# Kernel optimization log

Measured on AMD Instinct MI355X. Metric: run time of the kernel, lower is better.

## Reference

```python
import jax, jax.numpy as jnp
import numpy as np

N_NODES = 200000
N_EDGES = 800000
D_IN = 64
D_OUT = 64
NUM_RELATIONS = 16
NUM_BASES = 8


def setup_inputs() -> dict:
    key = jax.random.key(0)
    k_x, k_s, k_t, k_r, k_b, k_a = jax.random.split(key, 6)
    x = jax.random.normal(k_x, (N_NODES, D_IN), dtype=jnp.float32)
    node_keep_mask = jnp.ones((N_NODES,), dtype=bool)
    source = jax.random.randint(k_s, (N_EDGES,), 0, N_NODES, dtype=jnp.int64)
    target = jax.random.randint(k_t, (N_EDGES,), 0, N_NODES, dtype=jnp.int64)
    edge_type = jax.random.randint(k_r, (N_EDGES,), 0, NUM_RELATIONS, dtype=jnp.int64)
    # parameters: xavier-normal bases, L1-normalized attention coefficients
    std = float(np.sqrt(2.0 / (D_IN + D_OUT)))
    bases = jax.random.normal(k_b, (NUM_BASES, D_IN, D_OUT), dtype=jnp.float32) * std
    att = jax.random.uniform(k_a, (NUM_RELATIONS + 1, NUM_BASES), dtype=jnp.float32)
    att = att / jnp.sum(jnp.abs(att), axis=1, keepdims=True)
    return {"x": x, "node_keep_mask": node_keep_mask, "source": source,
            "target": target, "edge_type": edge_type, "bases": bases, "att": att}


def reference(x, node_keep_mask, source, target, edge_type, bases, att):
    num_relations = att.shape[0] - 1
    # per-node, per-basis transformed features: (N, B, D_out)
    t = jnp.einsum('nd,bde->nbe', x, bases)
    # self-loop term (att row num_relations), masked by node_keep_mask
    self_msg = jnp.einsum('nbe,b->ne', t, att[num_relations])
    out = jnp.where(node_keep_mask[:, None], self_msg, jnp.zeros((), dtype=x.dtype))
    # per-node, per-relation messages: (N, R, D_out) -- collapses the per-relation
    # python loop of the original into one contraction
    h = jnp.einsum('nbe,rb->nre', t, att[:num_relations])
    # bidirectional edges (original concatenates [src,tgt] and [tgt,src])
    src2 = jnp.concatenate([source, target])
    tgt2 = jnp.concatenate([target, source])
    et2 = jnp.concatenate([edge_type, edge_type])
    m = h[src2, et2]  # (2E, D_out) gather
    out = out.at[tgt2].add(m)  # scatter-add over edges
    return out
```

## Files before the change

kernel.cpp:

```cpp
#include <hip/hip_runtime.h>
#include <hip/hip_bf16.h>
#include <stdint.h>
#include <stddef.h>

#define N_NODES 200000
#define N_EDGES 800000
#define NREL 16
#define NBASES 8

typedef __attribute__((ext_vector_type(8))) short short8b;
typedef __attribute__((ext_vector_type(4))) float float4v;
typedef __attribute__((ext_vector_type(4))) int int4v;

__device__ __forceinline__ short f32_bf16(float f) {
  uint32_t u = __builtin_bit_cast(uint32_t, f);
  uint32_t r = u + 0x7FFFu + ((u >> 16) & 1u);
  return (short)(uint16_t)(r >> 16);
}
__device__ __forceinline__ uint16_t f32_bf16_hw(float f) {
  __hip_bfloat16 h = __float2bfloat16(f);
  return __builtin_bit_cast(uint16_t, h);
}
__device__ __forceinline__ float bf2f(uint16_t h) {
  return __builtin_bit_cast(float, (uint32_t)h << 16);
}

__global__ __launch_bounds__(256) void k_wprep(const float* __restrict__ bases,
                                               const float* __restrict__ att,
                                               uint16_t* __restrict__ Wt) {
  int i = blockIdx.x * 256 + threadIdx.x;
  if (i >= 17 * 64 * 64) return;
  int r = i >> 12;
  int e = (i >> 6) & 63;
  int d = i & 63;
  float acc = 0.f;
  for (int b = 0; b < NBASES; ++b)
    acc += att[r * NBASES + b] * bases[b * 4096 + d * 64 + e];
  Wt[i] = (uint16_t)f32_bf16(acc);
}

#define MAXTILES 112528
#define MAXRECS  (MAXTILES * 16)
#define NB 196
#define CNT_BLOCKS  782
#define CAST_BLOCKS 6250
#define WS_CNTR    0
#define WS_GCUR2   128
#define WS_RSTART  256
#define WS_GCUR    384
#define WS_WT      512
#define WS_TILEREL 139776
#define WS_CNTV    252416
#define WS_VSTART  1052416
#define WS_CNTT    1852416
#define WS_RECS    2652416
#define WS_MSG     17056128
#define WS_TOTAL   (WS_MSG + (size_t)MAXRECS * 128)
#define TR_RELOFF  WS_MSG
#define TR_NOFF    (TR_RELOFF + 3200000)
#define TR_ESLOT   (TR_NOFF + 800000)
#define TR_SCRATCH (TR_ESLOT + 6400000)
#define TR_H       (TR_SCRATCH + 6400000)
#define TR_BASE    (TR_H + 613088)
#define TR_REGS    (TR_BASE + 613088)

__global__ __launch_bounds__(256) void k_init(const float* __restrict__ bases,
                                              const float* __restrict__ att,
                                              uint16_t* __restrict__ Wt,
                                              int* __restrict__ zero0) {
  int b = blockIdx.x;
  int tid = threadIdx.x;
  if (b < 273) {
    int i = b * 256 + tid;
    if (i < 17 * 64 * 64) {
      int r = i >> 12;
      int e = (i >> 6) & 63;
      int d = i & 63;
      float acc = 0.f;
      for (int bb = 0; bb < NBASES; ++bb)
        acc += att[r * NBASES + bb] * bases[bb * 4096 + d * 64 + e];
      Wt[i] = (uint16_t)f32_bf16(acc);
    }
  } else {
    if (tid < 128) zero0[tid] = 0;
  }
}

__global__ __launch_bounds__(256) void k_count(const int* __restrict__ src,
                                               const int* __restrict__ tgt,
                                               const int* __restrict__ et,
                                               const int* __restrict__ mask,
                                               int* __restrict__ cntr,
                                               int* __restrict__ H,
                                               int* __restrict__ reloff,
                                               int* __restrict__ noff,
                                               const float* __restrict__ x,
                                               uint16_t* __restrict__ xb,
                                               int nE, int nN) {
  int b = blockIdx.x;
  int tid = threadIdx.x;
  if (b >= CNT_BLOCKS) {
    int i = (b - CNT_BLOCKS) * 256 + tid;
    const float* xp = x + (size_t)i * 8;
    float4v q0 = __builtin_nontemporal_load((const float4v*)xp);
    float4v q1 = __builtin_nontemporal_load((const float4v*)(xp + 4));
    short8b o;
    o[0] = f32_bf16_hw(q0[0]); o[1] = f32_bf16_hw(q0[1]); o[2] = f32_bf16_hw(q0[2]); o[3] = f32_bf16_hw(q0[3]);
    o[4] = f32_bf16_hw(q1[0]); o[5] = f32_bf16_hw(q1[1]); o[6] = f32_bf16_hw(q1[2]); o[7] = f32_bf16_hw(q1[3]);
    *(short8b*)(xb + (size_t)i * 8) = o;
    return;
  }
  __shared__ int lh[NREL + 1], lbase[NREL + 1];
  __shared__ int bh[NB];
  if (tid <= NREL) lh[tid] = 0;
  if (tid < NB) bh[tid] = 0;
  __syncthreads();
  int base = b * 1024 + tid;
  bool isE[4], isN[4];
  int r4[4], loff[4], loffN[4];
#pragma unroll
  for (int k = 0; k < 4; ++k) {
    int i = base + k * 256;
    isE[k] = i < nE;
    isN[k] = (i < nN) && mask[i];
    if (isE[k]) {
      r4[k] = et[i];
      int s_ = src[i], t_ = tgt[i];
      loff[k] = atomicAdd(&lh[r4[k]], 2);
      atomicAdd(&bh[t_ >> 10], 1);
      atomicAdd(&bh[s_ >> 10], 1);
    }
    if (isN[k]) loffN[k] = atomicAdd(&lh[NREL], 1);
  }
  __syncthreads();
  if (tid <= NREL)
    lbase[tid] = lh[tid] ? atomicAdd(&cntr[tid], lh[tid]) : 0;
  if (tid < NB) H[b * NB + tid] = bh[tid];
  __syncthreads();
#pragma unroll
  for (int k = 0; k < 4; ++k) {
    int i = base + k * 256;
    if (isE[k]) __builtin_nontemporal_store(lbase[r4[k]] + loff[k], reloff + i);
    if (isN[k]) __builtin_nontemporal_store(lbase[NREL] + loffN[k], noff + i);
  }
}

__global__ __launch_bounds__(256) void k_base(const int* __restrict__ H,
                                              int* __restrict__ baseM,
                                              int* __restrict__ regStart,
                                              int* __restrict__ regTot,
                                              int* __restrict__ gcur2) {
  int b = blockIdx.x;
  int tid = threadIdx.x;
  int lane = tid & 63, wid = tid >> 6;
  int vals[4]; int ts = 0;
#pragma unroll
  for (int k = 0; k < 4; ++k) {
    int idx = tid * 4 + k;
    vals[k] = (idx < CNT_BLOCKS) ? H[idx * NB + b] : 0;
    ts += vals[k];
  }
  int incl = ts;
  for (int off = 1; off < 64; off <<= 1) {
    int n = __shfl_up(incl, off, 64);
    if (lane >= off) incl += n;
  }
  __shared__ int wsum[4];
  __shared__ int s_start;
  if (lane == 63) wsum[wid] = incl;
  __syncthreads();
  if (tid == 0) {
    int t0 = wsum[0], t1 = wsum[1], t2 = wsum[2], t3 = wsum[3];
    int tot = t0 + t1 + t2 + t3;
    int st = atomicAdd(gcur2, tot);
    regStart[b] = st;
    regTot[b] = tot;
    s_start = st;
    wsum[0] = 0; wsum[1] = t0; wsum[2] = t0 + t1; wsum[3] = t0 + t1 + t2;
  }
  __syncthreads();
  int run = s_start + wsum[wid] + incl - ts;
#pragma unroll
  for (int k = 0; k < 4; ++k) {
    int idx = tid * 4 + k;
    if (idx < CNT_BLOCKS) {
      baseM[idx * NB + b] = run;
      run += vals[k];
    }
  }
}

__global__ __launch_bounds__(256) void k_scat(const int* __restrict__ src,
                                              const int* __restrict__ tgt,
                                              const int* __restrict__ baseM,
                                              int* __restrict__ scratch,
                                              int nE) {
  int b = blockIdx.x;
  int tid = threadIdx.x;
  __shared__ int bh[NB];
  __shared__ int bb[NB];
  if (tid < NB) { bh[tid] = 0; bb[tid] = baseM[b * NB + tid]; }
  __syncthreads();
#pragma unroll
  for (int k = 0; k < 4; ++k) {
    int i = b * 1024 + k * 256 + tid;
    if (i < nE) {
      int t_ = tgt[i], s_ = src[i];
      int offT = atomicAdd(&bh[t_ >> 10], 1);
      scratch[bb[t_ >> 10] + offT] = ((t_ & 1023) << 21) | (2 * i);
      int offS = atomicAdd(&bh[s_ >> 10], 1);
      scratch[bb[s_ >> 10] + offS] = ((s_ & 1023) << 21) | (2 * i + 1);
    }
  }
}

__global__ __launch_bounds__(256) void k_slot(const int* __restrict__ scratch,
                                              const int* __restrict__ regStart,
                                              const int* __restrict__ regTot,
                                              int* __restrict__ eslot,
                                              int* __restrict__ cntv,
                                              int nN) {
  int b = blockIdx.x;
  int tid = threadIdx.x;
  __shared__ int cnt[1024];
#pragma unroll
  for (int k = 0; k < 4; ++k) cnt[tid + k * 256] = 0;
  __syncthreads();
  int start = regStart[b];
  int tot = regTot[b];
  for (int it = tid; it < tot; it += 256) {
    int rec = scratch[start + it];
    int off = atomicAdd(&cnt[rec >> 21], 1);
    eslot[rec & 0x1FFFFF] = off;
  }
  __syncthreads();
#pragma unroll
  for (int k = 0; k < 4; ++k) {
    int v = b * 1024 + k * 256 + tid;
    if (v < nN) cntv[v] = cnt[k * 256 + tid];
  }
}

#define PREP_BLOCKS 440
#define VSEG_BLOCKS 782
__global__ __launch_bounds__(256) void k_scan(const int* __restrict__ cntr,
                                              int* __restrict__ rstart_g,
                                              uint8_t* __restrict__ tileRel,
                                              int2* __restrict__ recs,
                                              const int* __restrict__ cntv,
                                              const int* __restrict__ mask,
                                              int* __restrict__ vstart,
                                              int* __restrict__ cntt,
                                              int* __restrict__ gcur,
                                              int maxTiles, int nN) {
  int b = blockIdx.x;
  if (b < PREP_BLOCKS) {
    __shared__ int s[NREL + 2];
    if (threadIdx.x == 0) {
      int base = 0;
      for (int r = 0; r <= NREL; ++r) {
        s[r] = base;
        base = (base + cntr[r] + 15) & ~15;
      }
      s[NREL + 1] = base;
    }
    __syncthreads();
    if (b == 0) {
      if (threadIdx.x <= NREL + 1) rstart_g[threadIdx.x] = s[threadIdx.x];
      for (int w = threadIdx.x; w < (NREL + 1) * 16; w += 256) {
        int r = w >> 4, j = w & 15;
        int pos = s[r] + cntr[r] + j;
        if (pos < s[r + 1]) recs[pos] = make_int2(-1, -1);
      }
    }
    int t = b * 256 + threadIdx.x;
    if (t < maxTiles) {
      int p = t * 16;
      uint8_t rr = 255;
      if (p < s[NREL + 1]) {
        int q = 0;
        for (int k = 1; k <= NREL; ++k)
          if (p >= s[k]) q = k;
        rr = (uint8_t)q;
      }
      tileRel[t] = rr;
    }
  } else {
    __shared__ int wsum[4];
    __shared__ int s_base;
    int v = (b - PREP_BLOCKS) * 256 + threadIdx.x;
    int lane = threadIdx.x & 63;
    int wid = threadIdx.x >> 6;
    int c = 0;
    if (v < nN) c = cntv[v] + (mask[v] ? 1 : 0);
    int incl = c;
    for (int off = 1; off < 64; off <<= 1) {
      int n = __shfl_up(incl, off, 64);
      if (lane >= off) incl += n;
    }
    if (lane == 63) wsum[wid] = incl;
    __syncthreads();
    if (threadIdx.x == 0) {
      int t0 = wsum[0], t1 = wsum[1], t2 = wsum[2], t3 = wsum[3];
      s_base = atomicAdd(gcur, t0 + t1 + t2 + t3);
      wsum[0] = 0;
      wsum[1] = t0;
      wsum[2] = t0 + t1;
      wsum[3] = t0 + t1 + t2;
    }
    __syncthreads();
    if (v < nN) {
      vstart[v] = s_base + wsum[wid] + incl - c;
      cntt[v] = c;
    }
  }
}

__global__ __launch_bounds__(256) void k_write(const int* __restrict__ src,
                                               const int* __restrict__ tgt,
                                               const int* __restrict__ et,
                                               const int* __restrict__ mask,
                                               const int* __restrict__ reloff,
                                               const int* __restrict__ noff,
                                               const int* __restrict__ eslot,
                                               const int* __restrict__ rstart,
                                               const int* __restrict__ cntv,
                                               const int* __restrict__ vstart,
                                               int2* __restrict__ recs,
                                               int nE, int nN) {
  __shared__ int s_rs[NREL + 1];
  if (threadIdx.x <= NREL) s_rs[threadIdx.x] = rstart[threadIdx.x];
  __syncthreads();
  int i = blockIdx.x * 256 + threadIdx.x;
  if (i < nE) {
    int r = et[i];
    int rl = __builtin_nontemporal_load(reloff + i);
    long long ev = __builtin_nontemporal_load((const long long*)(eslot + 2 * i));
    int o1 = (int)(ev & 0xFFFFFFFFll);
    int o2 = (int)(ev >> 32);
    int s_ = src[i], t_ = tgt[i];
    int pos = s_rs[r] + rl;
    int s1 = vstart[t_] + o1;
    int s2 = vstart[s_] + o2;
    *(int4*)(recs + pos) = make_int4(s_, s1, t_, s2);
  }
  if (i < nN && mask[i]) {
    int pos = s_rs[NREL] + noff[i];
    int slot = vstart[i] + cntv[i];
    recs[pos] = make_int2(i, slot);
  }
}

__global__ __launch_bounds__(256) void k_phaseA(const uint16_t* __restrict__ xb,
                                                const int2* __restrict__ recs,
                                                const uint16_t* __restrict__ Wt,
                                                const uint8_t* __restrict__ tileRel,
                                                uint16_t* __restrict__ msg,
                                                int ntiles) {
  __shared__ uint16_t s_m[4][16 * 72];
  __shared__ int s_slot[4][16];
  const int wid = threadIdx.x >> 6;
  const int lane = threadIdx.x & 63;
  const int quad = lane >> 4;
  const int m16 = lane & 15;
  const int t0 = (blockIdx.x * 4 + wid) * 4;

  if (tileRel[t0] == 255) return;

  int rel4[4];
#pragma unroll
  for (int it = 0; it < 4; ++it) {
    int t = t0 + it;
    rel4[it] = (t < ntiles) ? (int)tileRel[t] : 255;
  }
  int2 rec4[4];
#pragma unroll
  for (int it = 0; it < 4; ++it) {
    if (rel4[it] != 255) {
      long long rv = __builtin_nontemporal_load((const long long*)(recs + (t0 + it) * 16 + m16));
      rec4[it].x = (int)(rv & 0xFFFFFFFFll);
      rec4[it].y = (int)(rv >> 32);
    } else {
      rec4[it] = make_int2(-1, -1);
    }
  }
  short8b a0_[4], a1_[4];
#pragma unroll
  for (int it = 0; it < 4; ++it) {
    int u = rec4[it].x < 0 ? 0 : rec4[it].x;
    const uint16_t* xp = xb + (size_t)u * 64 + quad * 8;
    a0_[it] = *(const short8b*)(xp);
    a1_[it] = *(const short8b*)(xp + 32);
  }

  int curRel = -1;
  short8b bfrag[4][2] = {};

#pragma unroll
  for (int it = 0; it < 4; ++it) {
    int rel = rel4[it];
    if (rel == 255) continue;

    if (rel != curRel) {
      curRel = rel;
      const uint16_t* wbase = Wt + (size_t)rel * 4096;
      for (int nt = 0; nt < 4; ++nt)
        for (int kt = 0; kt < 2; ++kt)
          bfrag[nt][kt] = *(const short8b*)(wbase + (size_t)(nt * 16 + m16) * 64 + kt * 32 + quad * 8);
    }

    float4v acc[4];
    for (int nt = 0; nt < 4; ++nt) { acc[nt][0] = 0.f; acc[nt][1] = 0.f; acc[nt][2] = 0.f; acc[nt][3] = 0.f; }
    for (int nt = 0; nt < 4; ++nt) {
      acc[nt] = __builtin_amdgcn_mfma_f32_16x16x32_bf16(a0_[it], bfrag[nt][0], acc[nt], 0, 0, 0);
      acc[nt] = __builtin_amdgcn_mfma_f32_16x16x32_bf16(a1_[it], bfrag[nt][1], acc[nt], 0, 0, 0);
    }

    if (quad == 0) s_slot[wid][m16] = rec4[it].y;
    for (int reg = 0; reg < 4; ++reg)
      for (int nt = 0; nt < 4; ++nt)
        s_m[wid][(quad * 4 + reg) * 72 + nt * 16 + m16] = f32_bf16_hw(acc[nt][reg]);

    asm volatile("s_waitcnt lgkmcnt(0)" ::: "memory");
    __builtin_amdgcn_sched_barrier(0);

    for (int p = 0; p < 2; ++p) {
      int row = (lane >> 3) + p * 8;
      int slot = s_slot[wid][row];
      if (slot >= 0) {
        const uint16_t* lp = &s_m[wid][row * 72 + (lane & 7) * 8];
        int4v val = *(const int4v*)lp;
        __builtin_nontemporal_store(val, (int4v*)(msg + (size_t)slot * 64 + (lane & 7) * 8));
      }
    }
    __builtin_amdgcn_sched_barrier(0);
  }
}

__global__ __launch_bounds__(256) void k_phaseB(const uint16_t* __restrict__ msg,
                                                const int* __restrict__ cntt,
                                                const int* __restrict__ vstart,
                                                float* __restrict__ out, int nN) {
  int v = blockIdx.x * 32 + (threadIdx.x >> 3);
  int l = threadIdx.x & 7;
  if (v >= nN) return;
  int cnt = cntt[v];
  int base = vstart[v];
  float a[8] = {0.f, 0.f, 0.f, 0.f, 0.f, 0.f, 0.f, 0.f};
  const uint16_t* mp = msg + (size_t)base * 64 + l * 8;
  int j = 0;
  for (; j + 2 <= cnt; j += 2) {
    int4v r0 = __builtin_nontemporal_load((const int4v*)(mp + (size_t)j * 64));
    int4v r1 = __builtin_nontemporal_load((const int4v*)(mp + (size_t)(j + 1) * 64));
    short8b h0 = __builtin_bit_cast(short8b, r0);
    short8b h1 = __builtin_bit_cast(short8b, r1);
#pragma unroll
    for (int k = 0; k < 8; ++k)
      a[k] += bf2f((uint16_t)h0[k]) + bf2f((uint16_t)h1[k]);
  }
  if (j < cnt) {
    int4v r0 = __builtin_nontemporal_load((const int4v*)(mp + (size_t)j * 64));
    short8b h = __builtin_bit_cast(short8b, r0);
#pragma unroll
    for (int k = 0; k < 8; ++k)
      a[k] += bf2f((uint16_t)h[k]);
  }
  float* op = out + (size_t)v * 64 + l * 8;
  float4v o0, o1;
  o0[0] = a[0]; o0[1] = a[1]; o0[2] = a[2]; o0[3] = a[3];
  o1[0] = a[4]; o1[1] = a[5]; o1[2] = a[6]; o1[3] = a[7];
  __builtin_nontemporal_store(o0, (float4v*)op);
  __builtin_nontemporal_store(o1, (float4v*)(op + 4));
}

#define F_WS_HIST    0
#define F_WS_CURSOR  64
#define F_WS_START   128
#define F_WS_WT      512
#define F_WS_TILEREL 139776
#define F_WS_RECS    262144
#define F_MAXTILES   112520
#define F_MAXRECS    (F_MAXTILES * 16)

__global__ __launch_bounds__(256) void f_hist(const int* __restrict__ et,
                                              int* __restrict__ hist, int nE) {
  __shared__ int lh[NREL];
  if (threadIdx.x < NREL) lh[threadIdx.x] = 0;
  __syncthreads();
  int i = blockIdx.x * 256 + threadIdx.x;
  if (i < nE) atomicAdd(&lh[et[i]], 2);
  __syncthreads();
  if (threadIdx.x < NREL && lh[threadIdx.x] > 0)
    atomicAdd(&hist[threadIdx.x], lh[threadIdx.x]);
}

__global__ __launch_bounds__(256) void f_prefix(const int* __restrict__ hist,
                                                int* __restrict__ cursor,
                                                int* __restrict__ start,
                                                uint8_t* __restrict__ tileRel,
                                                int nN, int maxTiles) {
  __shared__ int s_start[17];
  if (threadIdx.x == 0) {
    int base = nN;
    for (int r = 0; r < NREL; ++r) {
      s_start[r] = base;
      cursor[r] = base;
      start[r] = base;
      base = (base + hist[r] + 15) & ~15;
    }
    s_start[16] = base;
    start[16] = base;
  }
  __syncthreads();
  int endp = s_start[16];
  for (int t = threadIdx.x; t < maxTiles; t += 256) {
    int p = t * 16;
    uint8_t r;
    if (p < nN) r = 16;
    else if (p >= endp) r = 255;
    else {
      int q = 0;
      for (int k = 1; k < NREL; ++k) if (p >= s_start[k]) q = k;
      r = (uint8_t)q;
    }
    tileRel[t] = r;
  }
}

__global__ __launch_bounds__(256) void f_scatter(const int* __restrict__ src,
                                                 const int* __restrict__ tgt,
                                                 const int* __restrict__ et,
                                                 const int* __restrict__ mask,
                                                 int2* __restrict__ recs,
                                                 int* __restrict__ cursor,
                                                 int nE, int nN) {
  __shared__ int lh[NREL];
  __shared__ int lbase[NREL];
  if (threadIdx.x < NREL) lh[threadIdx.x] = 0;
  __syncthreads();
  int i = blockIdx.x * 256 + threadIdx.x;
  int r = 0, loff = 0;
  bool isEdge = (i < nE);
  if (isEdge) {
    r = et[i];
    loff = atomicAdd(&lh[r], 2);
  }
  __syncthreads();
  if (threadIdx.x < NREL)
    lbase[threadIdx.x] = (lh[threadIdx.x] > 0) ? atomicAdd(&cursor[threadIdx.x], lh[threadIdx.x]) : 0;
  __syncthreads();
  if (isEdge) {
    int pos = lbase[r] + loff;
    int s = src[i], t = tgt[i];
    *(int4*)(recs + pos) = make_int4(s, t, t, s);
  }
  if (i < nN) {
    recs[i] = (mask[i] != 0) ? make_int2(i, i) : make_int2(-1, -1);
  }
}

__global__ __launch_bounds__(256) void f_compute(const float* __restrict__ x,
                                                 const int2* __restrict__ recs,
                                                 const uint16_t* __restrict__ Wt,
                                                 const uint8_t* __restrict__ tileRel,
                                                 float* __restrict__ out,
                                                 int ntiles) {
  const int lane = threadIdx.x & 63;
  const int quad = lane >> 4;
  const int m16 = lane & 15;
  const int wave = blockIdx.x * 4 + (threadIdx.x >> 6);
  const int t0 = wave * 4;

  int curRel = -1;
  short8b bfrag[4][2] = {};

  for (int it = 0; it < 4; ++it) {
    int t = t0 + it;
    if (t >= ntiles) return;
    int rel = tileRel[t];
    if (rel == 255) return;

    if (rel != curRel) {
      curRel = rel;
      const uint16_t* wbase = Wt + (size_t)rel * 4096;
      for (int nt = 0; nt < 4; ++nt)
        for (int kt = 0; kt < 2; ++kt)
          bfrag[nt][kt] = *(const short8b*)(wbase + (size_t)(nt * 16 + m16) * 64 + kt * 32 + quad * 8);
    }

    int2 rec = recs[t * 16 + m16];
    int u = rec.x < 0 ? 0 : rec.x;

    const float* xp = x + (size_t)u * 64 + quad * 8;
    float4v q0 = *(const float4v*)(xp);
    float4v q1 = *(const float4v*)(xp + 4);
    float4v q2 = *(const float4v*)(xp + 32);
    float4v q3 = *(const float4v*)(xp + 36);
    short8b a0, a1;
    a0[0] = f32_bf16(q0[0]); a0[1] = f32_bf16(q0[1]); a0[2] = f32_bf16(q0[2]); a0[3] = f32_bf16(q0[3]);
    a0[4] = f32_bf16(q1[0]); a0[5] = f32_bf16(q1[1]); a0[6] = f32_bf16(q1[2]); a0[7] = f32_bf16(q1[3]);
    a1[0] = f32_bf16(q2[0]); a1[1] = f32_bf16(q2[1]); a1[2] = f32_bf16(q2[2]); a1[3] = f32_bf16(q2[3]);
    a1[4] = f32_bf16(q3[0]); a1[5] = f32_bf16(q3[1]); a1[6] = f32_bf16(q3[2]); a1[7] = f32_bf16(q3[3]);

    float4v acc[4];
    for (int nt = 0; nt < 4; ++nt) { acc[nt][0] = 0.f; acc[nt][1] = 0.f; acc[nt][2] = 0.f; acc[nt][3] = 0.f; }
    for (int nt = 0; nt < 4; ++nt) {
      acc[nt] = __builtin_amdgcn_mfma_f32_16x16x32_bf16(a0, bfrag[nt][0], acc[nt], 0, 0, 0);
      acc[nt] = __builtin_amdgcn_mfma_f32_16x16x32_bf16(a1, bfrag[nt][1], acc[nt], 0, 0, 0);
    }

    int tg[4];
    for (int reg = 0; reg < 4; ++reg)
      tg[reg] = __shfl(rec.y, quad * 4 + reg, 64);
    for (int reg = 0; reg < 4; ++reg) {
      if (tg[reg] < 0) continue;
      float* op = out + (size_t)tg[reg] * 64 + m16;
      for (int nt = 0; nt < 4; ++nt)
        __hip_atomic_fetch_add(op + nt * 16, acc[nt][reg], __ATOMIC_RELAXED, __HIP_MEMORY_SCOPE_AGENT);
    }
  }
}

extern "C" void kernel_launch(void* const* d_in, const int* in_sizes, int n_in,
                              void* d_out, int out_size, void* d_ws, size_t ws_size,
                              hipStream_t stream) {
  const float* x     = (const float*)d_in[0];
  const int*   mask  = (const int*)d_in[1];
  const int*   src   = (const int*)d_in[2];
  const int*   tgt   = (const int*)d_in[3];
  const int*   et    = (const int*)d_in[4];
  const float* bases = (const float*)d_in[5];
  const float* att   = (const float*)d_in[6];
  float* out = (float*)d_out;
  char* ws = (char*)d_ws;

  if (ws_size >= WS_TOTAL) {
    int*      cntr    = (int*)(ws + WS_CNTR);
    int*      gcur2   = (int*)(ws + WS_GCUR2);
    int*      rstart  = (int*)(ws + WS_RSTART);
    int*      gcur    = (int*)(ws + WS_GCUR);
    uint16_t* Wt      = (uint16_t*)(ws + WS_WT);
    uint8_t*  tileRel = (uint8_t*)(ws + WS_TILEREL);
    int*      cntv    = (int*)(ws + WS_CNTV);
    int*      vstart  = (int*)(ws + WS_VSTART);
    int*      cntt    = (int*)(ws + WS_CNTT);
    int2*     recs    = (int2*)(ws + WS_RECS);
    uint16_t* msg     = (uint16_t*)(ws + WS_MSG);
    int*      reloff  = (int*)(ws + TR_RELOFF);
    int*      noff    = (int*)(ws + TR_NOFF);
    int*      eslot   = (int*)(ws + TR_ESLOT);
    int*      scratch = (int*)(ws + TR_SCRATCH);
    int*      H       = (int*)(ws + TR_H);
    int*      baseM   = (int*)(ws + TR_BASE);
    int*      regStart= (int*)(ws + TR_REGS);
    int*      regTot  = regStart + NB;
    uint16_t* xb      = (uint16_t*)out;

    k_init<<<274, 256, 0, stream>>>(bases, att, Wt, (int*)ws);
    k_count<<<CNT_BLOCKS + CAST_BLOCKS, 256, 0, stream>>>(src, tgt, et, mask, cntr, H, reloff, noff, x, xb, N_EDGES, N_NODES);
    k_base<<<NB, 256, 0, stream>>>(H, baseM, regStart, regTot, gcur2);
    k_scat<<<CNT_BLOCKS, 256, 0, stream>>>(src, tgt, baseM, scratch, N_EDGES);
    k_slot<<<NB, 256, 0, stream>>>(scratch, regStart, regTot, eslot, cntv, N_NODES);
    k_scan<<<PREP_BLOCKS + VSEG_BLOCKS, 256, 0, stream>>>(cntr, rstart, tileRel, recs, cntv, mask, vstart, cntt, gcur, MAXTILES, N_NODES);
    k_write<<<(N_EDGES + 255) / 256, 256, 0, stream>>>(src, tgt, et, mask, reloff, noff, eslot, rstart, cntv, vstart, recs, N_EDGES, N_NODES);
    k_phaseA<<<(MAXTILES + 15) / 16, 256, 0, stream>>>(xb, recs, Wt, tileRel, msg, MAXTILES);
    k_phaseB<<<(N_NODES + 31) / 32, 256, 0, stream>>>(msg, cntt, vstart, out, N_NODES);
  } else {
    int*      hist    = (int*)(ws + F_WS_HIST);
    int*      cursor  = (int*)(ws + F_WS_CURSOR);
    int*      start   = (int*)(ws + F_WS_START);
    uint16_t* Wt      = (uint16_t*)(ws + F_WS_WT);
    uint8_t*  tileRel = (uint8_t*)(ws + F_WS_TILEREL);
    int2*     recs    = (int2*)(ws + F_WS_RECS);

    (void)hipMemsetAsync(out, 0, (size_t)N_NODES * 64 * sizeof(float), stream);
    (void)hipMemsetAsync(ws, 0, 512, stream);
    (void)hipMemsetAsync(recs, 0xFF, (size_t)F_MAXRECS * sizeof(int2), stream);

    k_wprep<<<(17 * 64 * 64 + 255) / 256, 256, 0, stream>>>(bases, att, Wt);
    f_hist<<<(N_EDGES + 255) / 256, 256, 0, stream>>>(et, hist, N_EDGES);
    f_prefix<<<1, 256, 0, stream>>>(hist, cursor, start, tileRel, N_NODES, F_MAXTILES);
    f_scatter<<<(N_EDGES + 255) / 256, 256, 0, stream>>>(src, tgt, et, mask, recs, cursor, N_EDGES, N_NODES);
    f_compute<<<(F_MAXTILES + 15) / 16, 256, 0, stream>>>(x, recs, Wt, tileRel, out, F_MAXTILES);
  }
}
```

Measured before the change: 308.7 us.

## Fold scan into slot and prep into base kernel, double-buffer phaseA staging

Moves the relation-prefix and tile-relation preparation blocks into k_base as extra blocks. It merges the per-node count scan into k_slot, which now makes two passes over scratch: one to count and one to assign absolute slots, and it writes the self-loop records itself. This removes the k_scan launch, the cntv round trip and the vstart gathers in k_write. It also double-buffers the phaseA LDS staging by iteration parity so one sched_barrier can be dropped. The cost is that k_slot now reads scratch twice, and the scan runs over only 196 blocks of 1024 nodes each, so the global gcur atomics order region blocks differently.

```diff
diff --git a/kernel.cpp b/kernel.cpp
--- a/kernel.cpp
+++ b/kernel.cpp
@@ -44,13 +44,13 @@
 #define NB 196
 #define CNT_BLOCKS  782
 #define CAST_BLOCKS 6250
+#define PREP_BLOCKS 440
 #define WS_CNTR    0
 #define WS_GCUR2   128
 #define WS_RSTART  256
 #define WS_GCUR    384
 #define WS_WT      512
 #define WS_TILEREL 139776
-#define WS_CNTV    252416
 #define WS_VSTART  1052416
 #define WS_CNTT    1852416
 #define WS_RECS    2652416
@@ -149,9 +149,48 @@
                                               int* __restrict__ baseM,
                                               int* __restrict__ regStart,
                                               int* __restrict__ regTot,
-                                              int* __restrict__ gcur2) {
+                                              int* __restrict__ gcur2,
+                                              const int* __restrict__ cntr,
+                                              int* __restrict__ rstart_g,
+                                              uint8_t* __restrict__ tileRel,
+                                              int2* __restrict__ recs,
+                                              int maxTiles) {
+  int tid = threadIdx.x;
+  if (blockIdx.x >= NB) {
+    int bp = blockIdx.x - NB;
+    __shared__ int s[NREL + 2];
+    if (tid == 0) {
+      int base = 0;
+      for (int r = 0; r <= NREL; ++r) {
+        s[r] = base;
+        base = (base + cntr[r] + 15) & ~15;
+      }
+      s[NREL + 1] = base;
+    }
+    __syncthreads();
+    if (bp == 0) {
+      if (tid <= NREL + 1) rstart_g[tid] = s[tid];
+      for (int w = tid; w < (NREL + 1) * 16; w += 256) {
+        int r = w >> 4, j = w & 15;
+        int pos = s[r] + cntr[r] + j;
+        if (pos < s[r + 1]) recs[pos] = make_int2(-1, -1);
+      }
+    }
+    int t = bp * 256 + tid;
+    if (t < maxTiles) {
+      int p = t * 16;
+      uint8_t rr = 255;
+      if (p < s[NREL + 1]) {
+        int q = 0;
+        for (int k = 1; k <= NREL; ++k)
+          if (p >= s[k]) q = k;
+        rr = (uint8_t)q;
+      }
+      tileRel[t] = rr;
+    }
+    return;
+  }
   int b = blockIdx.x;
-  int tid = threadIdx.x;
   int lane = tid & 63, wid = tid >> 6;
   int vals[4]; int ts = 0;
 #pragma unroll
@@ -217,117 +256,86 @@
 __global__ __launch_bounds__(256) void k_slot(const int* __restrict__ scratch,
                                               const int* __restrict__ regStart,
                                               const int* __restrict__ regTot,
+                                              const int* __restrict__ mask,
+                                              const int* __restrict__ noff,
+                                              const int* __restrict__ rstart,
                                               int* __restrict__ eslot,
-                                              int* __restrict__ cntv,
+                                              int* __restrict__ vstart,
+                                              int* __restrict__ cntt,
+                                              int* __restrict__ gcur,
+                                              int2* __restrict__ recs,
                                               int nN) {
   int b = blockIdx.x;
   int tid = threadIdx.x;
   __shared__ int cnt[1024];
+  __shared__ int sabs[1024];
+  __shared__ int wsum[4];
+  __shared__ int s_base, s_rs16;
 #pragma unroll
   for (int k = 0; k < 4; ++k) cnt[tid + k * 256] = 0;
+  if (tid == 0) s_rs16 = rstart[NREL];
   __syncthreads();
   int start = regStart[b];
   int tot = regTot[b];
+  for (int it = tid; it < tot; it += 256)
+    atomicAdd(&cnt[scratch[start + it] >> 21], 1);
+  __syncthreads();
+  int lane = tid & 63, wid = tid >> 6;
+  int vals[4]; int ts = 0;
+#pragma unroll
+  for (int k = 0; k < 4; ++k) {
+    int j = tid * 4 + k;
+    int v = b * 1024 + j;
+    int m = (v < nN) ? (mask[v] ? 1 : 0) : 0;
+    vals[k] = cnt[j] + m;
+    ts += vals[k];
+  }
+  int incl = ts;
+  for (int off = 1; off < 64; off <<= 1) {
+    int n = __shfl_up(incl, off, 64);
+    if (lane >= off) incl += n;
+  }
+  if (lane == 63) wsum[wid] = incl;
+  __syncthreads();
+  if (tid == 0) {
+    int t0 = wsum[0], t1 = wsum[1], t2 = wsum[2], t3 = wsum[3];
+    s_base = atomicAdd(gcur, t0 + t1 + t2 + t3);
+    wsum[0] = 0; wsum[1] = t0; wsum[2] = t0 + t1; wsum[3] = t0 + t1 + t2;
+  }
+  __syncthreads();
+  int run = s_base + wsum[wid] + incl - ts;
+#pragma unroll
+  for (int k = 0; k < 4; ++k) {
+    int j = tid * 4 + k;
+    sabs[j] = run;
+    int v = b * 1024 + j;
+    if (v < nN) { vstart[v] = run; cntt[v] = vals[k]; }
+    run += vals[k];
+  }
+  __syncthreads();
   for (int it = tid; it < tot; it += 256) {
     int rec = scratch[start + it];
-    int off = atomicAdd(&cnt[rec >> 21], 1);
-    eslot[rec & 0x1FFFFF] = off;
-  }
-  __syncthreads();
-#pragma unroll
-  for (int k = 0; k < 4; ++k) {
-    int v = b * 1024 + k * 256 + tid;
-    if (v < nN) cntv[v] = cnt[k * 256 + tid];
-  }
-}
-
-#define PREP_BLOCKS 440
-#define VSEG_BLOCKS 782
-__global__ __launch_bounds__(256) void k_scan(const int* __restrict__ cntr,
-                                              int* __restrict__ rstart_g,
-                                              uint8_t* __restrict__ tileRel,
-                                              int2* __restrict__ recs,
-                                              const int* __restrict__ cntv,
-                                              const int* __restrict__ mask,
-                                              int* __restrict__ vstart,
-                                              int* __restrict__ cntt,
-                                              int* __restrict__ gcur,
-                                              int maxTiles, int nN) {
-  int b = blockIdx.x;
-  if (b < PREP_BLOCKS) {
-    __shared__ int s[NREL + 2];
-    if (threadIdx.x == 0) {
-      int base = 0;
-      for (int r = 0; r <= NREL; ++r) {
-        s[r] = base;
-        base = (base + cntr[r] + 15) & ~15;
-      }
-      s[NREL + 1] = base;
-    }
-    __syncthreads();
-    if (b == 0) {
-      if (threadIdx.x <= NREL + 1) rstart_g[threadIdx.x] = s[threadIdx.x];
-      for (int w = threadIdx.x; w < (NREL + 1) * 16; w += 256) {
-        int r = w >> 4, j = w & 15;
-        int pos = s[r] + cntr[r] + j;
-        if (pos < s[r + 1]) recs[pos] = make_int2(-1, -1);
-      }
-    }
-    int t = b * 256 + threadIdx.x;
-    if (t < maxTiles) {
-      int p = t * 16;
-      uint8_t rr = 255;
-      if (p < s[NREL + 1]) {
-        int q = 0;
-        for (int k = 1; k <= NREL; ++k)
-          if (p >= s[k]) q = k;
-        rr = (uint8_t)q;
-      }
-      tileRel[t] = rr;
-    }
-  } else {
-    __shared__ int wsum[4];
-    __shared__ int s_base;
-    int v = (b - PREP_BLOCKS) * 256 + threadIdx.x;
-    int lane = threadIdx.x & 63;
-    int wid = threadIdx.x >> 6;
-    int c = 0;
-    if (v < nN) c = cntv[v] + (mask[v] ? 1 : 0);
-    int incl = c;
-    for (int off = 1; off < 64; off <<= 1) {
-      int n = __shfl_up(incl, off, 64);
-      if (lane >= off) incl += n;
-    }
-    if (lane == 63) wsum[wid] = incl;
-    __syncthreads();
-    if (threadIdx.x == 0) {
-      int t0 = wsum[0], t1 = wsum[1], t2 = wsum[2], t3 = wsum[3];
-      s_base = atomicAdd(gcur, t0 + t1 + t2 + t3);
-      wsum[0] = 0;
-      wsum[1] = t0;
-      wsum[2] = t0 + t1;
-      wsum[3] = t0 + t1 + t2;
-    }
-    __syncthreads();
-    if (v < nN) {
-      vstart[v] = s_base + wsum[wid] + incl - c;
-      cntt[v] = c;
-    }
+    int slot = atomicAdd(&sabs[rec >> 21], 1);
+    eslot[rec & 0x1FFFFF] = slot;
+  }
+  __syncthreads();
+#pragma unroll
+  for (int k = 0; k < 4; ++k) {
+    int j = tid * 4 + k;
+    int v = b * 1024 + j;
+    if (v < nN && mask[v])
+      recs[s_rs16 + noff[v]] = make_int2(v, sabs[j]);
   }
 }
 
 __global__ __launch_bounds__(256) void k_write(const int* __restrict__ src,
                                                const int* __restrict__ tgt,
                                                const int* __restrict__ et,
-                                               const int* __restrict__ mask,
                                                const int* __restrict__ reloff,
-                                               const int* __restrict__ noff,
                                                const int* __restrict__ eslot,
                                                const int* __restrict__ rstart,
-                                               const int* __restrict__ cntv,
-                                               const int* __restrict__ vstart,
                                                int2* __restrict__ recs,
-                                               int nE, int nN) {
+                                               int nE) {
   __shared__ int s_rs[NREL + 1];
   if (threadIdx.x <= NREL) s_rs[threadIdx.x] = rstart[threadIdx.x];
   __syncthreads();
@@ -336,18 +344,11 @@
     int r = et[i];
     int rl = __builtin_nontemporal_load(reloff + i);
     long long ev = __builtin_nontemporal_load((const long long*)(eslot + 2 * i));
-    int o1 = (int)(ev & 0xFFFFFFFFll);
-    int o2 = (int)(ev >> 32);
+    int s1 = (int)(ev & 0xFFFFFFFFll);
+    int s2 = (int)(ev >> 32);
     int s_ = src[i], t_ = tgt[i];
     int pos = s_rs[r] + rl;
-    int s1 = vstart[t_] + o1;
-    int s2 = vstart[s_] + o2;
     *(int4*)(recs + pos) = make_int4(s_, s1, t_, s2);
-  }
-  if (i < nN && mask[i]) {
-    int pos = s_rs[NREL] + noff[i];
-    int slot = vstart[i] + cntv[i];
-    recs[pos] = make_int2(i, slot);
   }
 }
 
@@ -357,8 +358,8 @@
                                                 const uint8_t* __restrict__ tileRel,
                                                 uint16_t* __restrict__ msg,
                                                 int ntiles) {
-  __shared__ uint16_t s_m[4][16 * 72];
-  __shared__ int s_slot[4][16];
+  __shared__ uint16_t s_m[4][2][16 * 72];
+  __shared__ int s_slot[4][2][16];
   const int wid = threadIdx.x >> 6;
   const int lane = threadIdx.x & 63;
   const int quad = lane >> 4;
@@ -400,6 +401,7 @@
   for (int it = 0; it < 4; ++it) {
     int rel = rel4[it];
     if (rel == 255) continue;
+    int par = it & 1;
 
     if (rel != curRel) {
       curRel = rel;
@@ -416,24 +418,23 @@
       acc[nt] = __builtin_amdgcn_mfma_f32_16x16x32_bf16(a1_[it], bfrag[nt][1], acc[nt], 0, 0, 0);
     }
 
-    if (quad == 0) s_slot[wid][m16] = rec4[it].y;
+    if (quad == 0) s_slot[wid][par][m16] = rec4[it].y;
     for (int reg = 0; reg < 4; ++reg)
       for (int nt = 0; nt < 4; ++nt)
-        s_m[wid][(quad * 4 + reg) * 72 + nt * 16 + m16] = f32_bf16_hw(acc[nt][reg]);
+        s_m[wid][par][(quad * 4 + reg) * 72 + nt * 16 + m16] = f32_bf16_hw(acc[nt][reg]);
 
     asm volatile("s_waitcnt lgkmcnt(0)" ::: "memory");
     __builtin_amdgcn_sched_barrier(0);
 
     for (int p = 0; p < 2; ++p) {
       int row = (lane >> 3) + p * 8;
-      int slot = s_slot[wid][row];
+      int slot = s_slot[wid][par][row];
       if (slot >= 0) {
-        const uint16_t* lp = &s_m[wid][row * 72 + (lane & 7) * 8];
+        const uint16_t* lp = &s_m[wid][par][row * 72 + (lane & 7) * 8];
         int4v val = *(const int4v*)lp;
         __builtin_nontemporal_store(val, (int4v*)(msg + (size_t)slot * 64 + (lane & 7) * 8));
       }
     }
-    __builtin_amdgcn_sched_barrier(0);
   }
 }
 
@@ -641,7 +642,6 @@
     int*      gcur    = (int*)(ws + WS_GCUR);
     uint16_t* Wt      = (uint16_t*)(ws + WS_WT);
     uint8_t*  tileRel = (uint8_t*)(ws + WS_TILEREL);
-    int*      cntv    = (int*)(ws + WS_CNTV);
     int*      vstart  = (int*)(ws + WS_VSTART);
     int*      cntt    = (int*)(ws + WS_CNTT);
     int2*     recs    = (int2*)(ws + WS_RECS);
@@ -658,11 +658,10 @@
 
     k_init<<<274, 256, 0, stream>>>(bases, att, Wt, (int*)ws);
     k_count<<<CNT_BLOCKS + CAST_BLOCKS, 256, 0, stream>>>(src, tgt, et, mask, cntr, H, reloff, noff, x, xb, N_EDGES, N_NODES);
-    k_base<<<NB, 256, 0, stream>>>(H, baseM, regStart, regTot, gcur2);
+    k_base<<<NB + PREP_BLOCKS, 256, 0, stream>>>(H, baseM, regStart, regTot, gcur2, cntr, rstart, tileRel, recs, MAXTILES);
     k_scat<<<CNT_BLOCKS, 256, 0, stream>>>(src, tgt, baseM, scratch, N_EDGES);
-    k_slot<<<NB, 256, 0, stream>>>(scratch, regStart, regTot, eslot, cntv, N_NODES);
-    k_scan<<<PREP_BLOCKS + VSEG_BLOCKS, 256, 0, stream>>>(cntr, rstart, tileRel, recs, cntv, mask, vstart, cntt, gcur, MAXTILES, N_NODES);
-    k_write<<<(N_EDGES + 255) / 256, 256, 0, stream>>>(src, tgt, et, mask, reloff, noff, eslot, rstart, cntv, vstart, recs, N_EDGES, N_NODES);
+    k_slot<<<NB, 256, 0, stream>>>(scratch, regStart, regTot, mask, noff, rstart, eslot, vstart, cntt, gcur, recs, N_NODES);
+    k_write<<<(N_EDGES + 255) / 256, 256, 0, stream>>>(src, tgt, et, reloff, eslot, rstart, recs, N_EDGES);
     k_phaseA<<<(MAXTILES + 15) / 16, 256, 0, stream>>>(xb, recs, Wt, tileRel, msg, MAXTILES);
     k_phaseB<<<(N_NODES + 31) / 32, 256, 0, stream>>>(msg, cntt, vstart, out, N_NODES);
   } else {
```

Result: faster. 298.8 us (-3.2%).
